# Kernel optimization log

Measured on AMD Instinct MI355X. Metric: run time of the kernel, lower is better.

Reference implementation:

```python
import jax, jax.numpy as jnp
import numpy as np

DIM_INPUTS = 64
HIDDEN = 256
LATENT = 64
SEQ_LEN = 128
BATCH = 4096


def _glorot(key, shape, fan_in):
    bound = 1.0 / np.sqrt(fan_in)
    return jax.random.uniform(key, shape, jnp.float32, -bound, bound)


def setup_inputs() -> dict:
    key = jax.random.key(0)
    ks = jax.random.split(key, 24)
    d, h, l = DIM_INPUTS, HIDDEN, LATENT
    inp = {
        "data": jax.random.normal(ks[0], (BATCH, SEQ_LEN, d), jnp.float32),
        "locs": jax.random.normal(ks[1], (BATCH, 2), jnp.float32),
        # LSTMCell params (torch layout: W_ih [4H, d], W_hh [4H, H], gate order i,f,g,o)
        "W_ih": _glorot(ks[2], (4 * h, d), h),
        "W_hh": _glorot(ks[3], (4 * h, h), h),
        "b_ih": _glorot(ks[4], (4 * h,), h),
        "b_hh": _glorot(ks[5], (4 * h,), h),
        "W_mu": _glorot(ks[6], (l, h), h), "b_mu": _glorot(ks[7], (l,), h),
        "W_var": _glorot(ks[8], (l, h), h), "b_var": _glorot(ks[9], (l,), h),
        "W_velo": _glorot(ks[10], (l, h), h), "b_velo": _glorot(ks[11], (l,), h),
        "W_switch": _glorot(ks[12], (l, h), h), "b_switch": _glorot(ks[13], (l,), h),
        "W_gen": _glorot(ks[14], (1, l), l), "b_gen": _glorot(ks[15], (1,), l),
        "W_on": _glorot(ks[16], (1, l), l), "b_on": _glorot(ks[17], (1,), l),
        "W_next": _glorot(ks[18], (d, l), l), "b_next": _glorot(ks[19], (d,), l),
        "W_loc": _glorot(ks[20], (h, 2), 2), "b_loc": _glorot(ks[21], (h,), 2),
        # pre-sampled reparameterization noise for all steps (seq_len-1 steps)
        "eps": jax.random.normal(ks[22], (SEQ_LEN - 1, BATCH, l), jnp.float32),
    }
    return inp


def _lstm_cell(x, h, c, W_ih, W_hh, b_ih, b_hh):
    gates = x @ W_ih.T + h @ W_hh.T + b_ih + b_hh  # [B, 4H]
    i, f, g, o = jnp.split(gates, 4, axis=-1)
    i, f, o = jax.nn.sigmoid(i), jax.nn.sigmoid(f), jax.nn.sigmoid(o)
    g = jnp.tanh(g)
    c_new = f * c + i * g
    h_new = o * jnp.tanh(c_new)
    return h_new, c_new


def _forward(data, locs, W_ih, W_hh, b_ih, b_hh, W_mu, b_mu, W_var, b_var,
             W_velo, b_velo, W_switch, b_switch, W_gen, b_gen, W_on, b_on,
             W_next, b_next, W_loc, b_loc, eps):
    B = data.shape[0]
    h0 = locs @ W_loc.T + b_loc
    c0 = jnp.zeros((B, HIDDEN), data.dtype)
    x0 = data[:, 0, :]

    def step(carry, eps_t):
        x, h, c = carry
        h, c = _lstm_cell(x, h, c, W_ih, W_hh, b_ih, b_hh)
        mu = h @ W_mu.T + b_mu
        logvar = h @ W_var.T + b_var
        velo = h @ W_velo.T + b_velo
        switch = h @ W_switch.T + b_switch
        z = eps_t * jnp.exp(0.5 * logvar) + mu
        # decode
        delta = z @ W_next.T + b_next  # [B, d]
        state = jnp.concatenate(
            [jnp.zeros((B, 1), x.dtype), x[:, 1:] + delta[:, 1:]], axis=1)
        state = jax.nn.relu(state)
        totals_pre = jnp.sum(state, axis=1)
        generate = jax.nn.relu(velo @ W_gen.T + b_gen)  # [B, 1]
        on_off = jnp.where((switch @ W_on.T + b_on) > 0.0, 1.0, 0.0)  # [B, 1]
        add = (generate * on_off)[:, 0]  # only first channel gets central=1
        state = state.at[:, 0].add(add)
        totals_post = jnp.sum(state, axis=1)
        return (state, h, c), (state, generate, on_off, totals_pre, totals_post)

    _, (states, gens, onoffs, t_pre, t_post) = jax.lax.scan(
        step, (x0, h0, c0), eps)
    # scan stacks along time axis 0 -> permute to batch-major
    states_t = jnp.transpose(states, (1, 0, 2))       # [B, T-1, d]
    gens_t = jnp.transpose(gens, (1, 0, 2))           # [B, T-1, 1]
    onoff_t = jnp.transpose(onoffs, (1, 0, 2))        # [B, T-1, 1]
    zero = jnp.zeros((1, B), data.dtype)
    totals_no_gen = jnp.concatenate([zero, t_pre], axis=0).T   # [B, T]
    totals_gen = jnp.concatenate([zero, t_post], axis=0).T     # [B, T]
    return states_t, gens_t, onoff_t, totals_no_gen, totals_gen


def reference(data, locs, W_ih, W_hh, b_ih, b_hh, W_mu, b_mu, W_var, b_var,
              W_velo, b_velo, W_switch, b_switch, W_gen, b_gen, W_on, b_on,
              W_next, b_next, W_loc, b_loc, eps):
    return _forward(data, locs, W_ih, W_hh, b_ih, b_hh, W_mu, b_mu, W_var,
                    b_var, W_velo, b_velo, W_switch, b_switch, W_gen, b_gen,
                    W_on, b_on, W_next, b_next, W_loc, b_loc, eps)
```

## Files before the change

kernel.cpp:

```cpp
#include <hip/hip_runtime.h>
#include <cmath>

#define T_STEPS 127
#define BATCHN  4096
#define DIN     64
#define SEQ     128

#define GBSH   327680
#define HBSH   131072
#define TOTSH  (GBSH + HBSH)
#define F0     (TOTSH / 2)
#define BG_F   F0
#define BH_F   (F0 + 1024)
#define WNP_F  (F0 + 1280)
#define F_END  (F0 + 5376)

#define O_STATES 0L
#define O_GENS   33292288L
#define O_ONOFF  33812480L
#define O_TNG    34332672L
#define O_TG     34856960L

#define P1SCALE   2048.0f
#define P1INV     4.8828125e-4f

typedef float    float4v __attribute__((ext_vector_type(4)));
typedef _Float16 f16x8   __attribute__((ext_vector_type(8)));

__device__ __forceinline__ float sigmoid_f(float x) {
    return 1.0f / (1.0f + __expf(-x));
}
__device__ __forceinline__ float tanh_f(float x) {
    float cx = fminf(15.0f, fmaxf(-15.0f, x));
    float e = __expf(2.0f * cx);
    return (e - 1.0f) / (e + 1.0f);
}
__device__ __forceinline__ void wave_sum64_3(float& a, float& b, float& c) {
    #pragma unroll
    for (int off = 32; off > 0; off >>= 1) {
        a += __shfl_xor(a, off, 64);
        b += __shfl_xor(b, off, 64);
        c += __shfl_xor(c, off, 64);
    }
}
__device__ __forceinline__ void f16x2_split(float v, _Float16& p0, _Float16& p1s) {
    p0 = (_Float16)v;
    float r = v - (float)p0;
    p1s = (_Float16)(r * P1SCALE);
}

__global__ void prep_kernel(const float* __restrict__ W_ih, const float* __restrict__ W_hh,
                            const float* __restrict__ b_ih, const float* __restrict__ b_hh,
                            const float* __restrict__ W_mu, const float* __restrict__ W_var,
                            const float* __restrict__ W_velo, const float* __restrict__ W_switch,
                            const float* __restrict__ b_mu, const float* __restrict__ b_var,
                            const float* __restrict__ b_velo, const float* __restrict__ b_switch,
                            const float* __restrict__ W_next, float* __restrict__ ws) {
    int idx = blockIdx.x * blockDim.x + threadIdx.x;
    int stride = gridDim.x * blockDim.x;

    _Float16* gh = (_Float16*)ws;

    for (int s = idx; s < GBSH; s += stride) {
        int j = s & 7, l = (s >> 3) & 63, tile = s >> 9;
        int ct = tile & 63, kt = tile >> 6;
        int n = ct * 16 + (l & 15);
        int k = kt * 32 + ((l >> 4) << 3) + j;
        float v = (k < 64) ? W_ih[n * 64 + k] : W_hh[n * 256 + (k - 64)];
        gh[s] = (_Float16)v;
    }

    for (int s = idx; s < HBSH; s += stride) {
        int j = s & 7, l = (s >> 3) & 63, r = s >> 9;
        int p = r & 1, tile = r >> 1, ct = tile & 15, kt = tile >> 4;
        int n = ct * 16 + (l & 15);
        int k = kt * 32 + ((l >> 4) << 3) + j;
        int hsel = n >> 6, jf = n & 63;
        const float* W = (hsel == 0) ? W_mu : (hsel == 1) ? W_var : (hsel == 2) ? W_velo : W_switch;
        float v = W[jf * 256 + k];
        _Float16 p0, p1s;
        f16x2_split(v, p0, p1s);
        gh[GBSH + s] = (p == 0) ? p0 : p1s;
    }

    for (int i = F0 + idx; i < F_END; i += stride) {
        float v;
        if (i < BH_F) {
            int n = i - BG_F;
            v = b_ih[n] + b_hh[n];
        } else if (i < WNP_F) {
            int c = i - BH_F;
            int hsel = c >> 6, jf = c & 63;
            const float* b = (hsel == 0) ? b_mu : (hsel == 1) ? b_var : (hsel == 2) ? b_velo : b_switch;
            v = b[jf];
        } else {
            int t = i - WNP_F;
            int kk = t & 3, jf = (t >> 2) & 63, kc = t >> 8;
            int k = kc * 4 + kk;
            v = W_next[jf * 64 + k];
        }
        ws[i] = v;
    }
}

__global__ __launch_bounds__(1024, 4)
void model_kernel(const float* __restrict__ data, const float* __restrict__ locs,
                  const float* __restrict__ W_loc, const float* __restrict__ b_loc,
                  const float* __restrict__ b_next, const float* __restrict__ W_gen,
                  const float* __restrict__ b_gen, const float* __restrict__ W_on,
                  const float* __restrict__ b_on, const float* __restrict__ eps,
                  const float* __restrict__ ws, float* __restrict__ out) {
    __shared__ __align__(16) float headbuf[4][16][68];
    __shared__ __align__(16) _Float16 af0[16][328];
    __shared__ __align__(16) _Float16 af1[16][328];
    __shared__ __align__(16) float wnl[4096];

    const int tid  = threadIdx.x;
    const int r0   = blockIdx.x * 16;
    const int w    = tid >> 6;
    const int ln   = tid & 63;
    const int ln15 = ln & 15;
    const int quad = ln >> 4;

    float x_reg;
    {
        float v = data[(size_t)(r0 + w) * SEQ * DIN + ln];
        x_reg = v;
        _Float16 p0, p1s; f16x2_split(v, p0, p1s);
        af0[w][ln] = p0; af1[w][ln] = p1s;
    }
    {
        int j = tid & 255, rh = tid >> 8;
        float w0 = W_loc[j * 2], w1 = W_loc[j * 2 + 1], bl = b_loc[j];
        #pragma unroll
        for (int rr = 0; rr < 4; ++rr) {
            int r = rh * 4 + rr;
            float hv = locs[(r0 + r) * 2] * w0 + locs[(r0 + r) * 2 + 1] * w1 + bl;
            _Float16 p0, p1s; f16x2_split(hv, p0, p1s);
            af0[r][64 + j] = p0; af1[r][64 + j] = p1s;
        }
    }
    for (int i = tid; i < 4096; i += 1024) wnl[i] = ws[WNP_F + i];
    if (tid < 16) {
        out[O_TNG + (long)(r0 + tid) * 128] = 0.0f;
        out[O_TG  + (long)(r0 + tid) * 128] = 0.0f;
    }
    __syncthreads();

    float c_st[4] = {0.0f, 0.0f, 0.0f, 0.0f};

    float bgc[4];
    #pragma unroll
    for (int g = 0; g < 4; ++g)
        bgc[g] = ws[BG_F + g * 256 + w * 16 + ln15];

    const float bhv  = ws[BH_F + w * 16 + ln15];
    const float bgen = b_gen[0];
    const float bon  = b_on[0];
    const float bnv  = b_next[ln];
    const float wgv  = W_gen[ln];
    const float wov  = W_on[ln];

    const f16x8* __restrict__ gb = (const f16x8*)ws;
    const f16x8* __restrict__ hb = gb + (GBSH / 8);

    for (int t = 0; t < T_STEPS; ++t) {
        const float ep = eps[((size_t)t * BATCHN + r0 + w) * 64 + ln];

        float4v acc1[4], acc2[4];
        #pragma unroll
        for (int g = 0; g < 4; ++g) {
            float b = bgc[g];
            acc1[g][0] = b; acc1[g][1] = b; acc1[g][2] = b; acc1[g][3] = b;
            acc2[g][0] = 0.0f; acc2[g][1] = 0.0f; acc2[g][2] = 0.0f; acc2[g][3] = 0.0f;
        }

        #pragma unroll 2
        for (int kt = 0; kt < 10; ++kt) {
            int ke = kt * 32 + quad * 8;
            f16x8 A0 = *(const f16x8*)&af0[ln15][ke];
            f16x8 A1 = *(const f16x8*)&af1[ln15][ke];
            int kbase = kt * 4096 + ln;
            #pragma unroll
            for (int g = 0; g < 4; ++g) {
                f16x8 B0 = gb[kbase + (g * 16 + w) * 64];
                acc1[g] = __builtin_amdgcn_mfma_f32_16x16x32_f16(A0, B0, acc1[g], 0, 0, 0);
                acc2[g] = __builtin_amdgcn_mfma_f32_16x16x32_f16(A1, B0, acc2[g], 0, 0, 0);
            }
        }

        float hval[4];
        #pragma unroll
        for (int rg = 0; rg < 4; ++rg) {
            float gi = fmaf(acc2[0][rg], P1INV, acc1[0][rg]);
            float gf = fmaf(acc2[1][rg], P1INV, acc1[1][rg]);
            float gg = fmaf(acc2[2][rg], P1INV, acc1[2][rg]);
            float go = fmaf(acc2[3][rg], P1INV, acc1[3][rg]);
            float iv = sigmoid_f(gi);
            float fv = sigmoid_f(gf);
            float gv = tanh_f(gg);
            float ov = sigmoid_f(go);
            float cn = fv * c_st[rg] + iv * gv;
            c_st[rg] = cn;
            hval[rg] = ov * tanh_f(cn);
        }
        __syncthreads();
        {
            int hcol = 64 + w * 16 + ln15;
            #pragma unroll
            for (int rg = 0; rg < 4; ++rg) {
                int row = quad * 4 + rg;
                _Float16 p0, p1s; f16x2_split(hval[rg], p0, p1s);
                af0[row][hcol] = p0;
                af1[row][hcol] = p1s;
            }
        }
        __syncthreads();

        {
            float4v hacc1, hacc2;
            hacc1[0] = bhv; hacc1[1] = bhv; hacc1[2] = bhv; hacc1[3] = bhv;
            hacc2[0] = 0.0f; hacc2[1] = 0.0f; hacc2[2] = 0.0f; hacc2[3] = 0.0f;
            #pragma unroll 2
            for (int kt = 0; kt < 8; ++kt) {
                int ke = 64 + kt * 32 + quad * 8;
                f16x8 A0 = *(const f16x8*)&af0[ln15][ke];
                f16x8 A1 = *(const f16x8*)&af1[ln15][ke];
                int idx = kt * 2048 + w * 128 + ln;
                f16x8 B0 = hb[idx];
                f16x8 B1 = hb[idx + 64];
                hacc1 = __builtin_amdgcn_mfma_f32_16x16x32_f16(A0, B0, hacc1, 0, 0, 0);
                hacc2 = __builtin_amdgcn_mfma_f32_16x16x32_f16(A0, B1, hacc2, 0, 0, 0);
                hacc2 = __builtin_amdgcn_mfma_f32_16x16x32_f16(A1, B0, hacc2, 0, 0, 0);
            }
            int n = w * 16 + ln15, hsel = n >> 6, f2 = n & 63;
            #pragma unroll
            for (int rg = 0; rg < 4; ++rg)
                headbuf[hsel][quad * 4 + rg][f2] = fmaf(hacc2[rg], P1INV, hacc1[rg]);
        }
        __syncthreads();

        headbuf[0][w][ln] = ep * __expf(0.5f * headbuf[1][w][ln]) + headbuf[0][w][ln];

        {
            float dacc = bnv;
            #pragma unroll 4
            for (int kc = 0; kc < 16; ++kc) {
                float4 cw = *(const float4*)&wnl[(kc * 64 + ln) * 4];
                float4 zv = *(const float4*)&headbuf[0][w][kc * 4];
                dacc = fmaf(zv.x, cw.x, fmaf(zv.y, cw.y, fmaf(zv.z, cw.z, fmaf(zv.w, cw.w, dacc))));
            }
            float sv = (ln == 0) ? 0.0f : fmaxf(x_reg + dacc, 0.0f);
            float sa = sv;
            float sb = headbuf[2][w][ln] * wgv;
            float sc = headbuf[3][w][ln] * wov;
            wave_sum64_3(sa, sb, sc);
            float gen = fmaxf(sb + bgen, 0.0f);
            float onf = (sc + bon > 0.0f) ? 1.0f : 0.0f;
            float add = gen * onf;
            if (ln == 0) sv = add;
            float tpost = sa + add;
            out[O_STATES + (long)(r0 + w) * (127L * 64) + (long)t * 64 + ln] = sv;
            x_reg = sv;
            _Float16 p0, p1s; f16x2_split(sv, p0, p1s);
            af0[w][ln] = p0; af1[w][ln] = p1s;
            if (ln == 0) {
                long rb127 = (long)(r0 + w) * 127 + t;
                out[O_GENS  + rb127] = gen;
                out[O_ONOFF + rb127] = onf;
                long rb128 = (long)(r0 + w) * 128 + t + 1;
                out[O_TNG + rb128] = sa;
                out[O_TG  + rb128] = tpost;
            }
        }
        __syncthreads();
    }
}

extern "C" void kernel_launch(void* const* d_in, const int* in_sizes, int n_in,
                              void* d_out, int out_size, void* d_ws, size_t ws_size,
                              hipStream_t stream) {
    const float* data     = (const float*)d_in[0];
    const float* locs     = (const float*)d_in[1];
    const float* W_ih     = (const float*)d_in[2];
    const float* W_hh     = (const float*)d_in[3];
    const float* b_ih     = (const float*)d_in[4];
    const float* b_hh     = (const float*)d_in[5];
    const float* W_mu     = (const float*)d_in[6];
    const float* b_mu     = (const float*)d_in[7];
    const float* W_var    = (const float*)d_in[8];
    const float* b_var    = (const float*)d_in[9];
    const float* W_velo   = (const float*)d_in[10];
    const float* b_velo   = (const float*)d_in[11];
    const float* W_switch = (const float*)d_in[12];
    const float* b_switch = (const float*)d_in[13];
    const float* W_gen    = (const float*)d_in[14];
    const float* b_gen    = (const float*)d_in[15];
    const float* W_on     = (const float*)d_in[16];
    const float* b_on     = (const float*)d_in[17];
    const float* W_next   = (const float*)d_in[18];
    const float* b_next   = (const float*)d_in[19];
    const float* W_loc    = (const float*)d_in[20];
    const float* b_loc    = (const float*)d_in[21];
    const float* eps      = (const float*)d_in[22];

    float* ws  = (float*)d_ws;
    float* out = (float*)d_out;

    prep_kernel<<<256, 256, 0, stream>>>(W_ih, W_hh, b_ih, b_hh,
                                         W_mu, W_var, W_velo, W_switch,
                                         b_mu, b_var, b_velo, b_switch,
                                         W_next, ws);
    model_kernel<<<256, 1024, 0, stream>>>(data, locs, W_loc, b_loc, b_next,
                                           W_gen, b_gen, W_on, b_on, eps, ws, out);
}
```

Measured before the change: 1.817 ms.

## Drop split-f16 correction for gate GEMM, prefetch head weights, use rcp activations

Removes the second (residual) f16 MFMA pass for the LSTM gate GEMM, so the gates use a single f16 product with the x input stored only as a plain f16 value, which roughly halves gate MFMA work. The head weight fragments are loaded into registers early, half before the gate GEMM and half before the head GEMM, to hide global load latency. Sigmoid and tanh switch from divisions to hardware reciprocal. This lowers accuracy of the recurrent gate computation and raises register pressure.

New measurement: 1.822 ms. No clear change (+0.2%).

```diff
diff --git a/kernel.cpp b/kernel.cpp
--- a/kernel.cpp
+++ b/kernel.cpp
@@ -28,12 +28,13 @@
 typedef _Float16 f16x8   __attribute__((ext_vector_type(8)));
 
 __device__ __forceinline__ float sigmoid_f(float x) {
-    return 1.0f / (1.0f + __expf(-x));
+    float e = __expf(-x);
+    return __builtin_amdgcn_rcpf(1.0f + e);
 }
 __device__ __forceinline__ float tanh_f(float x) {
     float cx = fminf(15.0f, fmaxf(-15.0f, x));
     float e = __expf(2.0f * cx);
-    return (e - 1.0f) / (e + 1.0f);
+    return fmaf(-2.0f, __builtin_amdgcn_rcpf(e + 1.0f), 1.0f);
 }
 __device__ __forceinline__ void wave_sum64_3(float& a, float& b, float& c) {
     #pragma unroll
@@ -126,8 +127,7 @@
     {
         float v = data[(size_t)(r0 + w) * SEQ * DIN + ln];
         x_reg = v;
-        _Float16 p0, p1s; f16x2_split(v, p0, p1s);
-        af0[w][ln] = p0; af1[w][ln] = p1s;
+        af0[w][ln] = (_Float16)v;
     }
     {
         int j = tid & 255, rh = tid >> 8;
@@ -167,39 +167,40 @@
     for (int t = 0; t < T_STEPS; ++t) {
         const float ep = eps[((size_t)t * BATCHN + r0 + w) * 64 + ln];
 
-        float4v acc1[4], acc2[4];
+        f16x8 hbr[8];
+        #pragma unroll
+        for (int kt = 0; kt < 4; ++kt) {
+            int idx = kt * 2048 + w * 128 + ln;
+            hbr[2 * kt]     = hb[idx];
+            hbr[2 * kt + 1] = hb[idx + 64];
+        }
+
+        float4v acc1[4];
         #pragma unroll
         for (int g = 0; g < 4; ++g) {
             float b = bgc[g];
             acc1[g][0] = b; acc1[g][1] = b; acc1[g][2] = b; acc1[g][3] = b;
-            acc2[g][0] = 0.0f; acc2[g][1] = 0.0f; acc2[g][2] = 0.0f; acc2[g][3] = 0.0f;
         }
 
         #pragma unroll 2
         for (int kt = 0; kt < 10; ++kt) {
             int ke = kt * 32 + quad * 8;
             f16x8 A0 = *(const f16x8*)&af0[ln15][ke];
-            f16x8 A1 = *(const f16x8*)&af1[ln15][ke];
             int kbase = kt * 4096 + ln;
             #pragma unroll
             for (int g = 0; g < 4; ++g) {
                 f16x8 B0 = gb[kbase + (g * 16 + w) * 64];
                 acc1[g] = __builtin_amdgcn_mfma_f32_16x16x32_f16(A0, B0, acc1[g], 0, 0, 0);
-                acc2[g] = __builtin_amdgcn_mfma_f32_16x16x32_f16(A1, B0, acc2[g], 0, 0, 0);
             }
         }
 
         float hval[4];
         #pragma unroll
         for (int rg = 0; rg < 4; ++rg) {
-            float gi = fmaf(acc2[0][rg], P1INV, acc1[0][rg]);
-            float gf = fmaf(acc2[1][rg], P1INV, acc1[1][rg]);
-            float gg = fmaf(acc2[2][rg], P1INV, acc1[2][rg]);
-            float go = fmaf(acc2[3][rg], P1INV, acc1[3][rg]);
-            float iv = sigmoid_f(gi);
-            float fv = sigmoid_f(gf);
-            float gv = tanh_f(gg);
-            float ov = sigmoid_f(go);
+            float iv = sigmoid_f(acc1[0][rg]);
+            float fv = sigmoid_f(acc1[1][rg]);
+            float gv = tanh_f(acc1[2][rg]);
+            float ov = sigmoid_f(acc1[3][rg]);
             float cn = fv * c_st[rg] + iv * gv;
             c_st[rg] = cn;
             hval[rg] = ov * tanh_f(cn);
@@ -218,17 +219,23 @@
         __syncthreads();
 
         {
+            f16x8 t0[4], t1[4];
+            #pragma unroll
+            for (int kt2 = 0; kt2 < 4; ++kt2) {
+                int idx = (kt2 + 4) * 2048 + w * 128 + ln;
+                t0[kt2] = hb[idx];
+                t1[kt2] = hb[idx + 64];
+            }
             float4v hacc1, hacc2;
             hacc1[0] = bhv; hacc1[1] = bhv; hacc1[2] = bhv; hacc1[3] = bhv;
             hacc2[0] = 0.0f; hacc2[1] = 0.0f; hacc2[2] = 0.0f; hacc2[3] = 0.0f;
-            #pragma unroll 2
+            #pragma unroll
             for (int kt = 0; kt < 8; ++kt) {
                 int ke = 64 + kt * 32 + quad * 8;
                 f16x8 A0 = *(const f16x8*)&af0[ln15][ke];
                 f16x8 A1 = *(const f16x8*)&af1[ln15][ke];
-                int idx = kt * 2048 + w * 128 + ln;
-                f16x8 B0 = hb[idx];
-                f16x8 B1 = hb[idx + 64];
+                f16x8 B0 = (kt < 4) ? hbr[2 * kt]     : t0[kt - 4];
+                f16x8 B1 = (kt < 4) ? hbr[2 * kt + 1] : t1[kt - 4];
                 hacc1 = __builtin_amdgcn_mfma_f32_16x16x32_f16(A0, B0, hacc1, 0, 0, 0);
                 hacc2 = __builtin_amdgcn_mfma_f32_16x16x32_f16(A0, B1, hacc2, 0, 0, 0);
                 hacc2 = __builtin_amdgcn_mfma_f32_16x16x32_f16(A1, B0, hacc2, 0, 0, 0);
@@ -262,8 +269,7 @@
             float tpost = sa + add;
             out[O_STATES + (long)(r0 + w) * (127L * 64) + (long)t * 64 + ln] = sv;
             x_reg = sv;
-            _Float16 p0, p1s; f16x2_split(sv, p0, p1s);
-            af0[w][ln] = p0; af1[w][ln] = p1s;
+            af0[w][ln] = (_Float16)sv;
             if (ln == 0) {
                 long rb127 = (long)(r0 + w) * 127 + t;
                 out[O_GENS  + rb127] = gen;
```
